# Kernel tuning notes

Hardware: AMD Instinct MI355X
Metric: run time of the kernel (lower is better)

The kernel has to match this reference:

```python
import jax, jax.numpy as jnp
import numpy as np

B, S, D, H, P = 4, 4096, 1024, 8, 32
K = D // H  # head_dim = 128


def setup_inputs() -> dict:
    key = jax.random.key(0)
    ks = jax.random.split(key, 12)
    f = lambda k, shape, s: jax.random.normal(k, shape, dtype=jnp.float32) * s
    return {
        "x": f(ks[0], (B, S, D), 1.0),
        "W_proj": f(ks[1], (H, K, D), 0.03),
        "resonance_freqs": f(ks[2], (H, K), 0.01),
        "pol_W": f(ks[3], (H, P, K), 0.08),
        "pol_b": jnp.zeros((H, P), jnp.float32),
        "imp_W1": f(ks[4], (16, 1), 0.5),               # Linear(1, 16)
        "imp_b1": jnp.zeros((16,), jnp.float32),
        "imp_W2": f(ks[5], (1, 16), 0.25),              # Linear(16, 1)
        "imp_b2": jnp.zeros((1,), jnp.float32),
        "out_W": f(ks[6], (D, D), 0.03),                # Linear(dim, dim)
        "out_b": jnp.zeros((D,), jnp.float32),
        "ln_g": jnp.ones((D,), jnp.float32),
        "ln_b": jnp.zeros((D,), jnp.float32),
        "causal": 1,
    }


def reference(x, W_proj, resonance_freqs, pol_W, pol_b, imp_W1, imp_b1,
              imp_W2, imp_b2, out_W, out_b, ln_g, ln_b, causal):
    Bx, Sx, Dx = x.shape
    nH = W_proj.shape[0]
    # per-head projection + resonance frequency modulation -> (B, H, S, K)
    heads = jnp.einsum('bsd,hkd->bhsk', x, W_proj)
    heads = heads * jnp.cos(resonance_freqs * jnp.pi)[None, :, None, :]

    # --- GuaXiangDuiChong: learned cross-head impedance ---
    summary = heads.mean(axis=2)                                   # (B, H, K)
    pol = jnp.tanh(jnp.einsum('bhk,hpk->bhp', summary, pol_W) + pol_b[None])
    pol = pol / jnp.maximum(jnp.linalg.norm(pol, axis=-1, keepdims=True), 1e-12)
    dots = jnp.einsum('bhp,bgp->bhg', pol, pol)                    # (B, H, H)
    z = dots[..., None]                                            # (B, H, H, 1)
    hid = jax.nn.gelu(z * imp_W1[:, 0] + imp_b1, approximate=False)  # (B, H, H, 16)
    imp = jax.nn.softplus(jnp.einsum('bijc,oc->bijo', hid, imp_W2) + imp_b2)[..., 0]
    eye = jnp.eye(nH, dtype=x.dtype)
    impedance = imp * (1.0 - eye)                                  # (B, H, H)

    # --- cross-head transfer ---
    # h_i += sum_{j != i} heads_j / (1 + imp[i,j]) * 0.1, causally mean-masked.
    coef = (0.1 / (1.0 + impedance)) * (1.0 - eye)                 # zero diagonal (i == j skipped)
    transfer = jnp.einsum('bij,bjsk->bisk', coef, heads)           # (B, H, S, K)
    if causal and Sx > 1:
        # masked_fill(t>s)+mean over t of a key-independent tensor == scale by (s+1)/S
        scale = (jnp.arange(Sx, dtype=x.dtype) + 1.0) / Sx
        transfer = transfer * scale[None, None, :, None]
    out_heads = heads + transfer

    merged = out_heads.transpose(0, 2, 1, 3).reshape(Bx, Sx, Dx)   # cat heads on last dim
    y = merged @ out_W.T + out_b + x                               # dropout is identity in eval
    mu = y.mean(-1, keepdims=True)
    var = ((y - mu) ** 2).mean(-1, keepdims=True)
    normed = (y - mu) / jnp.sqrt(var + 1e-5) * ln_g + ln_b
    return normed, impedance
```

## Files before the change

kernel.cpp:

```cpp
#include <hip/hip_runtime.h>

typedef __bf16 bf16x8 __attribute__((ext_vector_type(8)));
typedef float f32x4 __attribute__((ext_vector_type(4)));
typedef unsigned short us8 __attribute__((ext_vector_type(8)));

#define PI_F 3.14159265358979323846f

__device__ __forceinline__ unsigned short f2bf(float f) {
    unsigned u = __float_as_uint(f);
    u += 0x7FFFu + ((u >> 16) & 1u);
    return (unsigned short)(u >> 16);
}
__device__ __forceinline__ float bf2f(unsigned short h) {
    return __uint_as_float(((unsigned)h) << 16);
}

__device__ __forceinline__ void async16(const void* g, void* l) {
    __builtin_amdgcn_global_load_lds(
        (const __attribute__((address_space(1))) unsigned int*)g,
        (__attribute__((address_space(3))) unsigned int*)l, 16, 0, 0);
}

__global__ __launch_bounds__(256) void prep_k(const float* __restrict__ W,
                                              const float* __restrict__ fr,
                                              const float* __restrict__ Wo,
                                              unsigned short* __restrict__ W1b,
                                              unsigned short* __restrict__ Wob) {
    int idx = blockIdx.x * 256 + threadIdx.x;
    if (idx < (1 << 20)) {
        int n = idx >> 10, d = idx & 1023;
        int k = n >> 3, h = n & 7;
        float c = cosf(fr[h * 128 + k] * PI_F);
        W1b[idx] = f2bf(W[((h * 128 + k) << 10) + d] * c);
    } else {
        int i2 = idx - (1 << 20);
        int n = i2 >> 10, dp = i2 & 1023;
        int k = dp >> 3, h = dp & 7;
        Wob[i2] = f2bf(Wo[(n << 10) + h * 128 + k]);
    }
}

__global__ __launch_bounds__(256) void xbar_cast(const float* __restrict__ x,
                                                 unsigned short* __restrict__ xb,
                                                 float* __restrict__ part) {
    int bid = blockIdx.x;
    int b = bid >> 8;
    int s0 = (bid & 255) * 16;
    int t = threadIdx.x;
    float a0 = 0.f, a1 = 0.f, a2 = 0.f, a3 = 0.f;
    for (int i = 0; i < 16; ++i) {
        long row = (long)b * 4096 + s0 + i;
        float4 v = ((const float4*)x)[row * 256 + t];
        a0 += v.x; a1 += v.y; a2 += v.z; a3 += v.w;
        ushort4 u;
        u.x = f2bf(v.x); u.y = f2bf(v.y); u.z = f2bf(v.z); u.w = f2bf(v.w);
        ((ushort4*)xb)[row * 256 + t] = u;
    }
    float4 p; p.x = a0; p.y = a1; p.z = a2; p.w = a3;
    ((float4*)part)[bid * 256 + t] = p;
}

__global__ __launch_bounds__(256) void xbar_r(const float* __restrict__ part,
                                              float* __restrict__ xbar) {
    __shared__ float sl[256];
    int blk = blockIdx.x;
    int b = blk >> 3, dgrp = blk & 7;
    int t = threadIdx.x;
    int col = dgrp * 128 + (t & 127);
    int ih = t >> 7;
    float s = 0.f;
    for (int i = 0; i < 128; ++i) {
        int cb = b * 256 + ih * 128 + i;
        s += part[cb * 1024 + col];
    }
    sl[t] = s;
    __syncthreads();
    if (t < 128) xbar[b * 1024 + col] = sl[t] + sl[t + 128];
}

__global__ __launch_bounds__(256) void summary_k(const float* __restrict__ xbar,
                                                 const float* __restrict__ W,
                                                 const float* __restrict__ fr,
                                                 float* __restrict__ summary) {
    int wave = (blockIdx.x * 256 + threadIdx.x) >> 6;
    int lane = threadIdx.x & 63;
    int b = wave >> 10, hk = wave & 1023;
    int h = hk >> 7, k = hk & 127;
    const float* wrow = &W[(h * 128 + k) << 10];
    const float* xrow = &xbar[b << 10];
    float s = 0.f;
    for (int d = lane; d < 1024; d += 64) s += xrow[d] * wrow[d];
    for (int off = 32; off; off >>= 1) s += __shfl_down(s, off);
    if (lane == 0) {
        float c = cosf(fr[h * 128 + k] * PI_F);
        summary[wave] = s * c * (1.0f / 4096.0f);
    }
}

__global__ __launch_bounds__(256) void imp_k(const float* __restrict__ summary,
                                             const float* __restrict__ pol_W,
                                             const float* __restrict__ pol_b,
                                             const float* __restrict__ imp_W1,
                                             const float* __restrict__ imp_b1,
                                             const float* __restrict__ imp_W2,
                                             const float* __restrict__ imp_b2,
                                             float* __restrict__ coef_out,
                                             float* __restrict__ imp_out) {
    __shared__ float pol[4][8][32];
    __shared__ float rn[32];
    int t = threadIdx.x;
    for (int o = t; o < 1024; o += 256) {
        int b = o >> 8, h = (o >> 5) & 7, p = o & 31;
        const float* srow = &summary[(b * 8 + h) * 128];
        const float* wrow = &pol_W[(h * 32 + p) * 128];
        float acc = pol_b[h * 32 + p];
        for (int k = 0; k < 128; ++k) acc += srow[k] * wrow[k];
        pol[b][h][p] = tanhf(acc);
    }
    __syncthreads();
    if (t < 32) {
        int b = t >> 3, h = t & 7;
        float ss = 0.f;
        for (int p = 0; p < 32; ++p) { float v = pol[b][h][p]; ss += v * v; }
        rn[t] = 1.0f / fmaxf(sqrtf(ss), 1e-12f);
    }
    __syncthreads();
    {
        int b = t >> 6, i = (t >> 3) & 7, j = t & 7;
        float d = 0.f;
        for (int p = 0; p < 32; ++p) d += pol[b][i][p] * pol[b][j][p];
        d *= rn[b * 8 + i] * rn[b * 8 + j];
        float s = imp_b2[0];
        for (int c = 0; c < 16; ++c) {
            float z = d * imp_W1[c] + imp_b1[c];
            float gl = 0.5f * z * (1.0f + erff(z * 0.70710678118654752f));
            s += gl * imp_W2[c];
        }
        float sp = fmaxf(s, 0.0f) + log1pf(expf(-fabsf(s)));
        float impv = (i == j) ? 0.0f : sp;
        imp_out[t] = impv;
        coef_out[t] = (i == j) ? 0.0f : 0.1f / (1.0f + impv);
    }
}

#define VMCNT(n) asm volatile("s_waitcnt vmcnt(" #n ")" ::: "memory")
#define SBAR() __builtin_amdgcn_s_barrier()

__device__ __forceinline__ void swizzle_blk(int n, long& rowBase, long& colBase) {
    int xcd = n & 7, s = n >> 3;
    rowBase = (long)(xcd * 16 + (s & 15)) * 128;
    colBase = (long)(s >> 4) * 128;
}

#define STG2(sPtr, dPtr, koff, slot)                                         \
    async16((sPtr) + (koff), (dPtr) + (slot) * 8192);                        \
    async16((sPtr) + (koff) + 131072, (dPtr) + (slot) * 8192 + 4096);

#define PH(p, DO_ST, KOFF, VM)                                               \
    {                                                                        \
        if (DO_ST) {                                                         \
            STG2(sA, stDstA, (KOFF), ((p) + 2) & 3)                          \
            STG2(sB, stDstB, (KOFF), ((p) + 2) & 3)                          \
        }                                                                    \
        VM;                                                                  \
        SBAR();                                                              \
        const char* pA = rdA + ((p) & 3) * 8192;                             \
        const char* pB = rdB + ((p) & 3) * 8192;                             \
        bf16x8 af[4], bv[4];                                                 \
        _Pragma("unroll") for (int i_ = 0; i_ < 4; ++i_)                     \
            af[i_] = *(const bf16x8*)(pA + i_ * 1024);                       \
        _Pragma("unroll") for (int i_ = 0; i_ < 4; ++i_)                     \
            bv[i_] = *(const bf16x8*)(pB + i_ * 1024);                       \
        __builtin_amdgcn_s_setprio(1);                                       \
        _Pragma("unroll") for (int mi = 0; mi < 4; ++mi)                     \
            _Pragma("unroll") for (int ni = 0; ni < 4; ++ni)                 \
                acc[mi][ni] = __builtin_amdgcn_mfma_f32_16x16x32_bf16(       \
                    af[mi], bv[ni], acc[mi][ni], 0, 0, 0);                   \
        __builtin_amdgcn_s_setprio(0);                                       \
    }

__device__ __forceinline__ void gemm4_core(const char* gAB, const char* gBB,
                                           char* smem, const int t,
                                           f32x4 acc[4][4]) {
    const int l = t & 63, wid = t >> 6;
    const int wm = wid >> 1, wn = wid & 1;
    const long stOff = (long)((wid << 4) + (t & 15)) * 2048 + ((t >> 4) & 3) * 16;
    const char* sA = gAB + stOff;
    const char* sB = gBB + stOff;
    char* As = smem;
    char* Bs = smem + 32768;
    char* stDstA = As + wid * 1024;
    char* stDstB = Bs + wid * 1024;
    const char* rdA = As + wm * 4096 + (l >> 4) * 256 + (l & 15) * 16;
    const char* rdB = Bs + wn * 4096 + (l >> 4) * 256 + (l & 15) * 16;

    STG2(sA, stDstA, 0, 0)
    STG2(sB, stDstB, 0, 0)
    STG2(sA, stDstA, 64, 1)
    STG2(sB, stDstB, 64, 1)

    int kb = 128;
    for (int grp = 0; grp < 7; ++grp) {
        PH(0, true, kb, VMCNT(8))
        PH(1, true, kb + 64, VMCNT(8))
        PH(2, true, kb + 128, VMCNT(8))
        PH(3, true, kb + 192, VMCNT(8))
        kb += 256;
    }
    PH(0, true, 1920, VMCNT(8))
    PH(1, true, 1984, VMCNT(8))
    PH(2, false, 0, VMCNT(4))
    PH(3, false, 0, VMCNT(0))
}

__global__ __launch_bounds__(256, 2) void gemm1_mix(
    const unsigned short* __restrict__ A, const unsigned short* __restrict__ B,
    const float* __restrict__ coef, const int* __restrict__ causal,
    unsigned short* __restrict__ C) {
    __shared__ char smem[65536];
    __shared__ float cfs[64];
    const int t = threadIdx.x;
    long rowBase, colBase;
    swizzle_blk(blockIdx.x, rowBase, colBase);
    const int b = (int)(rowBase >> 12);
    if (t < 64) cfs[t] = coef[b * 64 + t];
    const int causalv = causal[0];

    f32x4 acc[4][4] = {};
    gemm4_core((const char*)A + rowBase * 2048, (const char*)B + colBase * 2048,
               smem, t, acc);

    const int l = t & 63, wid = t >> 6;
    const int wm = wid >> 1, wn = wid & 1;
    const int q = l >> 4, c16 = l & 15;
    float* mixt = (float*)smem;
    const int r16 = t >> 4, kg = t & 15;
#pragma unroll
    for (int p = 0; p < 8; ++p) {
        if (wm == (p >> 2)) {
            int mi = p & 3;
#pragma unroll
            for (int ni = 0; ni < 4; ++ni)
#pragma unroll
                for (int r = 0; r < 4; ++r)
                    mixt[(q * 4 + r) * 132 + wn * 64 + ni * 16 + c16] = acc[mi][ni][r];
        }
        __syncthreads();
        const float* src = mixt + r16 * 132 + kg * 8;
        float v[8];
#pragma unroll
        for (int j = 0; j < 8; ++j) v[j] = src[j];
        long row = rowBase + p * 16 + r16;
        float scale = causalv ? (float)((row & 4095) + 1) * (1.0f / 4096.0f) : 1.0f;
        us8 o;
#pragma unroll
        for (int i = 0; i < 8; ++i) {
            float ts = 0.f;
#pragma unroll
            for (int j = 0; j < 8; ++j) ts += cfs[i * 8 + j] * v[j];
            o[i] = f2bf(v[i] + scale * ts);
        }
        *(us8*)(C + row * 1024 + colBase + kg * 8) = o;
        __syncthreads();
    }
}

__global__ __launch_bounds__(256, 2) void gemm_bt(const unsigned short* __restrict__ A,
                                                  const unsigned short* __restrict__ B,
                                                  unsigned short* __restrict__ C) {
    __shared__ char smem[65536];
    const int t = threadIdx.x;
    long rowBase, colBase;
    swizzle_blk(blockIdx.x, rowBase, colBase);

    f32x4 acc[4][4] = {};
    gemm4_core((const char*)A + rowBase * 2048, (const char*)B + colBase * 2048,
               smem, t, acc);

    const int l = t & 63, wid = t >> 6;
    const int wm = wid >> 1, wn = wid & 1;
    const int q = l >> 4, c16 = l & 15;
#pragma unroll
    for (int mi = 0; mi < 4; ++mi) {
#pragma unroll
        for (int ni = 0; ni < 4; ++ni) {
            long col = colBase + wn * 64 + ni * 16 + c16;
            long row0 = rowBase + wm * 64 + mi * 16 + q * 4;
#pragma unroll
            for (int r = 0; r < 4; ++r)
                C[(row0 + r) * 1024 + col] = f2bf(acc[mi][ni][r]);
        }
    }
}

__global__ __launch_bounds__(256) void ln_k(const unsigned short* __restrict__ ypre,
                                            const float* __restrict__ x,
                                            const float* __restrict__ outb,
                                            const float* __restrict__ gam,
                                            const float* __restrict__ bet,
                                            float* __restrict__ out) {
    int row = blockIdx.x;
    int t = threadIdx.x;
    long base = (long)row * 1024 + t * 4;
    ushort4 yp = *(const ushort4*)(ypre + base);
    float4 xv = *(const float4*)(x + base);
    float4 bv = *(const float4*)(outb + t * 4);
    float y0 = bf2f(yp.x) + xv.x + bv.x;
    float y1 = bf2f(yp.y) + xv.y + bv.y;
    float y2 = bf2f(yp.z) + xv.z + bv.z;
    float y3 = bf2f(yp.w) + xv.w + bv.w;
    float s = y0 + y1 + y2 + y3;
    float ss = y0 * y0 + y1 * y1 + y2 * y2 + y3 * y3;
    for (int off = 32; off; off >>= 1) {
        s += __shfl_down(s, off);
        ss += __shfl_down(ss, off);
    }
    __shared__ float red[8];
    int wv = t >> 6, ln = t & 63;
    if (ln == 0) { red[wv] = s; red[4 + wv] = ss; }
    __syncthreads();
    float S1 = red[0] + red[1] + red[2] + red[3];
    float S2 = red[4] + red[5] + red[6] + red[7];
    float mu = S1 * (1.0f / 1024.0f);
    float var = S2 * (1.0f / 1024.0f) - mu * mu;
    float rs = 1.0f / sqrtf(var + 1e-5f);
    float4 gv = *(const float4*)(gam + t * 4);
    float4 bb = *(const float4*)(bet + t * 4);
    float4 o;
    o.x = (y0 - mu) * rs * gv.x + bb.x;
    o.y = (y1 - mu) * rs * gv.y + bb.y;
    o.z = (y2 - mu) * rs * gv.z + bb.z;
    o.w = (y3 - mu) * rs * gv.w + bb.w;
    *(float4*)(out + base) = o;
}

extern "C" void kernel_launch(void* const* d_in, const int* in_sizes, int n_in,
                              void* d_out, int out_size, void* d_ws, size_t ws_size,
                              hipStream_t stream) {
    const float* x       = (const float*)d_in[0];
    const float* W_proj  = (const float*)d_in[1];
    const float* freqs   = (const float*)d_in[2];
    const float* pol_W   = (const float*)d_in[3];
    const float* pol_b   = (const float*)d_in[4];
    const float* imp_W1  = (const float*)d_in[5];
    const float* imp_b1  = (const float*)d_in[6];
    const float* imp_W2  = (const float*)d_in[7];
    const float* imp_b2  = (const float*)d_in[8];
    const float* out_W   = (const float*)d_in[9];
    const float* out_b   = (const float*)d_in[10];
    const float* ln_g    = (const float*)d_in[11];
    const float* ln_b    = (const float*)d_in[12];
    const int*   causal  = (const int*)d_in[13];
    float* out = (float*)d_out;

    char* ws = (char*)d_ws;
    unsigned short* xb      = (unsigned short*)(ws + 0);
    unsigned short* merged  = (unsigned short*)(ws + 33554432);
    unsigned short* w1b     = (unsigned short*)(ws + 67108864);
    unsigned short* wob     = (unsigned short*)(ws + 69206016);
    float* xbar             = (float*)(ws + 71303168);
    float* summary          = (float*)(ws + 71319552);
    float* coef             = (float*)(ws + 71335936);
    float* part             = (float*)merged;
    unsigned short* ypre    = xb;

    prep_k<<<8192, 256, 0, stream>>>(W_proj, freqs, out_W, w1b, wob);
    xbar_cast<<<1024, 256, 0, stream>>>(x, xb, part);
    xbar_r<<<32, 256, 0, stream>>>(part, xbar);
    summary_k<<<1024, 256, 0, stream>>>(xbar, W_proj, freqs, summary);
    imp_k<<<1, 256, 0, stream>>>(summary, pol_W, pol_b, imp_W1, imp_b1,
                                 imp_W2, imp_b2, coef, out + 16777216);
    gemm1_mix<<<1024, 256, 0, stream>>>(xb, w1b, coef, causal, merged);
    gemm_bt<<<1024, 256, 0, stream>>>(merged, wob, ypre);
    ln_k<<<16384, 256, 0, stream>>>(ypre, x, out_b, ln_g, ln_b, out);
}
```

Before: 338.7 us.

## Switch GEMMs to 128x256 tiles with 512 threads and double buffering

Both bf16 GEMMs now use 8 waves per block computing a 128x256 output tile instead of 4 waves on 128x128, which halves the grid and reuses each loaded A tile across twice as many columns. The LDS pipeline goes from a 4-slot ring with partial vmcnt waits to a 2-slot double buffer that waits for all loads to finish before each barrier. This reduces redundant global traffic for A, but it exposes load latency more because only one stage is in flight. The mix epilogue is widened to handle 256-column slabs.

After: 315.6 us. 1.07x faster.

```diff
diff --git a/kernel.cpp b/kernel.cpp
--- a/kernel.cpp
+++ b/kernel.cpp
@@ -146,26 +146,24 @@
 #define VMCNT(n) asm volatile("s_waitcnt vmcnt(" #n ")" ::: "memory")
 #define SBAR() __builtin_amdgcn_s_barrier()
 
-__device__ __forceinline__ void swizzle_blk(int n, long& rowBase, long& colBase) {
+__device__ __forceinline__ void swz512(int n, long& rowBase, long& colBase) {
     int xcd = n & 7, s = n >> 3;
     rowBase = (long)(xcd * 16 + (s & 15)) * 128;
-    colBase = (long)(s >> 4) * 128;
-}
-
-#define STG2(sPtr, dPtr, koff, slot)                                         \
-    async16((sPtr) + (koff), (dPtr) + (slot) * 8192);                        \
-    async16((sPtr) + (koff) + 131072, (dPtr) + (slot) * 8192 + 4096);
-
-#define PH(p, DO_ST, KOFF, VM)                                               \
+    colBase = (long)(s >> 4) * 256;
+}
+
+#define PH(p, DO_ST, KOFF)                                                   \
     {                                                                        \
+        VMCNT(0);                                                            \
+        SBAR();                                                              \
         if (DO_ST) {                                                         \
-            STG2(sA, stDstA, (KOFF), ((p) + 2) & 3)                          \
-            STG2(sB, stDstB, (KOFF), ((p) + 2) & 3)                          \
+            async16(sA + (KOFF), stDstA + (((p) + 1) & 1) * 8192);           \
+            async16(sB + (KOFF), stDstB + (((p) + 1) & 1) * 16384);          \
+            async16(sB + (KOFF) + 262144,                                    \
+                    stDstB + (((p) + 1) & 1) * 16384 + 8192);                \
         }                                                                    \
-        VM;                                                                  \
-        SBAR();                                                              \
-        const char* pA = rdA + ((p) & 3) * 8192;                             \
-        const char* pB = rdB + ((p) & 3) * 8192;                             \
+        const char* pA = rdA + ((p) & 1) * 8192;                             \
+        const char* pB = rdB + ((p) & 1) * 16384;                            \
         bf16x8 af[4], bv[4];                                                 \
         _Pragma("unroll") for (int i_ = 0; i_ < 4; ++i_)                     \
             af[i_] = *(const bf16x8*)(pA + i_ * 1024);                       \
@@ -179,79 +177,77 @@
         __builtin_amdgcn_s_setprio(0);                                       \
     }
 
-__device__ __forceinline__ void gemm4_core(const char* gAB, const char* gBB,
+__device__ __forceinline__ void gemm8_core(const char* gAB, const char* gBB,
                                            char* smem, const int t,
                                            f32x4 acc[4][4]) {
     const int l = t & 63, wid = t >> 6;
-    const int wm = wid >> 1, wn = wid & 1;
+    const int wm = wid >> 2, wn = wid & 3;
     const long stOff = (long)((wid << 4) + (t & 15)) * 2048 + ((t >> 4) & 3) * 16;
     const char* sA = gAB + stOff;
     const char* sB = gBB + stOff;
     char* As = smem;
-    char* Bs = smem + 32768;
+    char* Bs = smem + 16384;
     char* stDstA = As + wid * 1024;
     char* stDstB = Bs + wid * 1024;
     const char* rdA = As + wm * 4096 + (l >> 4) * 256 + (l & 15) * 16;
     const char* rdB = Bs + wn * 4096 + (l >> 4) * 256 + (l & 15) * 16;
 
-    STG2(sA, stDstA, 0, 0)
-    STG2(sB, stDstB, 0, 0)
-    STG2(sA, stDstA, 64, 1)
-    STG2(sB, stDstB, 64, 1)
-
-    int kb = 128;
-    for (int grp = 0; grp < 7; ++grp) {
-        PH(0, true, kb, VMCNT(8))
-        PH(1, true, kb + 64, VMCNT(8))
-        PH(2, true, kb + 128, VMCNT(8))
-        PH(3, true, kb + 192, VMCNT(8))
-        kb += 256;
-    }
-    PH(0, true, 1920, VMCNT(8))
-    PH(1, true, 1984, VMCNT(8))
-    PH(2, false, 0, VMCNT(4))
-    PH(3, false, 0, VMCNT(0))
-}
-
-__global__ __launch_bounds__(256, 2) void gemm1_mix(
+    async16(sA, stDstA);
+    async16(sB, stDstB);
+    async16(sB + 262144, stDstB + 8192);
+
+    int kb = 64;
+    for (int grp = 0; grp < 15; ++grp) {
+        PH(0, true, kb)
+        PH(1, true, kb + 64)
+        kb += 128;
+    }
+    PH(0, true, 1984)
+    PH(1, false, 0)
+}
+
+__global__ __launch_bounds__(512, 4) void gemm1_mix(
     const unsigned short* __restrict__ A, const unsigned short* __restrict__ B,
     const float* __restrict__ coef, const int* __restrict__ causal,
     unsigned short* __restrict__ C) {
-    __shared__ char smem[65536];
+    __shared__ char smem[49152];
     __shared__ float cfs[64];
     const int t = threadIdx.x;
     long rowBase, colBase;
-    swizzle_blk(blockIdx.x, rowBase, colBase);
+    swz512(blockIdx.x, rowBase, colBase);
     const int b = (int)(rowBase >> 12);
     if (t < 64) cfs[t] = coef[b * 64 + t];
     const int causalv = causal[0];
 
     f32x4 acc[4][4] = {};
-    gemm4_core((const char*)A + rowBase * 2048, (const char*)B + colBase * 2048,
+    gemm8_core((const char*)A + rowBase * 2048, (const char*)B + colBase * 2048,
                smem, t, acc);
+    __syncthreads();
 
     const int l = t & 63, wid = t >> 6;
-    const int wm = wid >> 1, wn = wid & 1;
+    const int wm = wid >> 2, wn = wid & 3;
     const int q = l >> 4, c16 = l & 15;
-    float* mixt = (float*)smem;
-    const int r16 = t >> 4, kg = t & 15;
+    float* slab = (float*)smem;
+    const int r16 = t >> 5, kg = t & 31;
 #pragma unroll
     for (int p = 0; p < 8; ++p) {
         if (wm == (p >> 2)) {
-            int mi = p & 3;
+            const int mi = p & 3;
 #pragma unroll
             for (int ni = 0; ni < 4; ++ni)
 #pragma unroll
                 for (int r = 0; r < 4; ++r)
-                    mixt[(q * 4 + r) * 132 + wn * 64 + ni * 16 + c16] = acc[mi][ni][r];
+                    slab[(q * 4 + r) * 264 + wn * 64 + ni * 16 + c16] =
+                        acc[mi][ni][r];
         }
         __syncthreads();
-        const float* src = mixt + r16 * 132 + kg * 8;
+        const float* src = slab + r16 * 264 + kg * 8;
         float v[8];
 #pragma unroll
         for (int j = 0; j < 8; ++j) v[j] = src[j];
-        long row = rowBase + p * 16 + r16;
-        float scale = causalv ? (float)((row & 4095) + 1) * (1.0f / 4096.0f) : 1.0f;
+        const long row = rowBase + p * 16 + r16;
+        const float scale =
+            causalv ? (float)((row & 4095) + 1) * (1.0f / 4096.0f) : 1.0f;
         us8 o;
 #pragma unroll
         for (int i = 0; i < 8; ++i) {
@@ -265,20 +261,20 @@
     }
 }
 
-__global__ __launch_bounds__(256, 2) void gemm_bt(const unsigned short* __restrict__ A,
+__global__ __launch_bounds__(512, 4) void gemm_bt(const unsigned short* __restrict__ A,
                                                   const unsigned short* __restrict__ B,
                                                   unsigned short* __restrict__ C) {
-    __shared__ char smem[65536];
+    __shared__ char smem[49152];
     const int t = threadIdx.x;
     long rowBase, colBase;
-    swizzle_blk(blockIdx.x, rowBase, colBase);
+    swz512(blockIdx.x, rowBase, colBase);
 
     f32x4 acc[4][4] = {};
-    gemm4_core((const char*)A + rowBase * 2048, (const char*)B + colBase * 2048,
+    gemm8_core((const char*)A + rowBase * 2048, (const char*)B + colBase * 2048,
                smem, t, acc);
 
     const int l = t & 63, wid = t >> 6;
-    const int wm = wid >> 1, wn = wid & 1;
+    const int wm = wid >> 2, wn = wid & 3;
     const int q = l >> 4, c16 = l & 15;
 #pragma unroll
     for (int mi = 0; mi < 4; ++mi) {
@@ -370,7 +366,7 @@
     summary_k<<<1024, 256, 0, stream>>>(xbar, W_proj, freqs, summary);
     imp_k<<<1, 256, 0, stream>>>(summary, pol_W, pol_b, imp_W1, imp_b1,
                                  imp_W2, imp_b2, coef, out + 16777216);
-    gemm1_mix<<<1024, 256, 0, stream>>>(xb, w1b, coef, causal, merged);
-    gemm_bt<<<1024, 256, 0, stream>>>(merged, wob, ypre);
+    gemm1_mix<<<512, 512, 0, stream>>>(xb, w1b, coef, causal, merged);
+    gemm_bt<<<512, 512, 0, stream>>>(merged, wob, ypre);
     ln_k<<<16384, 256, 0, stream>>>(ypre, x, out_b, ln_g, ln_b, out);
 }
```
